# Kernel tuning notes

Measured on AMD Instinct MI355X. Metric: run time of the kernel, lower is better.

Reference implementation:

```python
import jax, jax.numpy as jnp
import numpy as np

BATCH, SEQ, D_IN, D_OUT, PALETTE = 4, 2048, 4096, 4096, 256


def setup_inputs() -> dict:
    key = jax.random.key(0)
    k_in, k_w, k_lut, k_b = jax.random.split(key, 4)
    inp = jax.random.normal(k_in, (BATCH, SEQ, D_IN), dtype=jnp.float32)
    # palette indices playing the role of the stored uint8 weight tensor
    weight = jax.random.randint(k_w, (D_OUT, D_IN), 0, PALETTE, dtype=jnp.int32)
    # fp8-derived palette values (simulated as small fp32 centroids)
    lookup_table = jax.random.normal(k_lut, (PALETTE,), dtype=jnp.float32) * 0.02
    bias = jax.random.normal(k_b, (D_OUT,), dtype=jnp.float32) * 0.01
    return {"input": inp, "lookup_table": lookup_table, "weight": weight, "bias": bias}


def reference(input, lookup_table, weight, bias):
    # Dequantize palette indices -> full weight matrix [D_OUT, D_IN]
    full_weights = lookup_table[weight]
    # F.linear: input @ W^T + bias
    out = jnp.einsum("bsd,od->bso", input, full_weights)
    return out + bias
```

## Files before the change

### kernel.cpp

```cpp
#include <hip/hip_runtime.h>
#include <cstdint>


static constexpr int Md = 8192;
static constexpr int Nd = 4096;
static constexpr int Kd = 4096;
static constexpr int NKT = Kd / 64;

typedef _Float16 half8 __attribute__((ext_vector_type(8)));
typedef float f32x4 __attribute__((ext_vector_type(4)));

__device__ __forceinline__ void async_copy16(const _Float16* g, _Float16* l) {
  __builtin_amdgcn_global_load_lds((const __attribute__((address_space(1))) void*)g,
                                   (__attribute__((address_space(3))) void*)l, 16, 0, 0);
}

__global__ __launch_bounds__(256) void cvt_a(const float* __restrict__ in,
                                             _Float16* __restrict__ out) {
  const size_t i = (size_t)blockIdx.x * 256 + threadIdx.x;
  const float4 x = ((const float4*)in)[2 * i];
  const float4 y = ((const float4*)in)[2 * i + 1];
  half8 h;
  h[0] = (_Float16)x.x; h[1] = (_Float16)x.y; h[2] = (_Float16)x.z; h[3] = (_Float16)x.w;
  h[4] = (_Float16)y.x; h[5] = (_Float16)y.y; h[6] = (_Float16)y.z; h[7] = (_Float16)y.w;
  *(half8*)(out + 8 * i) = h;
}

__global__ __launch_bounds__(256) void dequant_b(const int* __restrict__ w,
                                                 const float* __restrict__ lut,
                                                 _Float16* __restrict__ out) {
  __shared__ float slut[256];
  slut[threadIdx.x] = lut[threadIdx.x];
  __syncthreads();
  const size_t i = (size_t)blockIdx.x * 256 + threadIdx.x;
  const int4 a = ((const int4*)w)[2 * i];
  const int4 b = ((const int4*)w)[2 * i + 1];
  half8 h;
  h[0] = (_Float16)slut[a.x]; h[1] = (_Float16)slut[a.y];
  h[2] = (_Float16)slut[a.z]; h[3] = (_Float16)slut[a.w];
  h[4] = (_Float16)slut[b.x]; h[5] = (_Float16)slut[b.y];
  h[6] = (_Float16)slut[b.z]; h[7] = (_Float16)slut[b.w];
  *(half8*)(out + 8 * i) = h;
}

__global__ __launch_bounds__(512, 2) void gemm_f16(const _Float16* __restrict__ A,
                                                   const _Float16* __restrict__ Bt,
                                                   const float* __restrict__ bias,
                                                   float* __restrict__ C) {
  __shared__ __align__(16) _Float16 As[2][256 * 64];
  __shared__ __align__(16) _Float16 Bs[2][256 * 64];

  const int tid = threadIdx.x;
  const int lane = tid & 63;
  const int wave = tid >> 6;
  const int wm = wave >> 2;
  const int wn = wave & 3;

  const int bid0 = blockIdx.x + blockIdx.y * gridDim.x;
  const int bid = (bid0 & 7) * 64 + (bid0 >> 3);
  const int bm = bid & 31;
  const int bn = bid >> 5;

  const int trow = tid >> 3;
  const int tcol = tid & 7;
  const int gch = tcol ^ (trow & 7);
  const _Float16* ag = A + (size_t)(bm * 256 + trow) * Kd + gch * 8;
  const _Float16* bg = Bt + (size_t)(bn * 256 + trow) * Kd + gch * 8;
  const int lds_off = trow * 64 + tcol * 8;

  auto stage = [&](int buf, int kt) {
#pragma unroll
    for (int ht = 0; ht < 4; ++ht) {
      async_copy16(ag + (size_t)kt * 64 + (size_t)ht * (64 * Kd),
                   &As[buf][lds_off + ht * 4096]);
      async_copy16(bg + (size_t)kt * 64 + (size_t)ht * (64 * Kd),
                   &Bs[buf][lds_off + ht * 4096]);
    }
  };

  const int fr = lane & 15;
  const int fq = lane >> 4;
  const int e = fr & 7;
  const int s0 = (fq ^ e) * 8;
  const int s1 = ((4 | fq) ^ e) * 8;

  f32x4 acc[8][4] = {};

  stage(0, 0);

  for (int kt = 0; kt < NKT; ++kt) {
    const int cur = kt & 1;
    if (kt + 1 < NKT) {
      stage(cur ^ 1, kt + 1);
      asm volatile("s_waitcnt vmcnt(8)" ::: "memory");
    } else {
      asm volatile("s_waitcnt vmcnt(0)" ::: "memory");
    }
    __builtin_amdgcn_s_barrier();

    const _Float16* as = &As[cur][(wm * 128 + fr) * 64];
    const _Float16* bs = &Bs[cur][(wn * 64 + fr) * 64];

    half8 a[4][2], b0[2][2], b1[2][2];

#pragma unroll
    for (int i = 0; i < 4; ++i) {
      a[i][0] = *(const half8*)(as + i * 16 * 64 + s0);
      a[i][1] = *(const half8*)(as + i * 16 * 64 + s1);
    }
#pragma unroll
    for (int j = 0; j < 2; ++j) {
      b0[j][0] = *(const half8*)(bs + j * 16 * 64 + s0);
      b0[j][1] = *(const half8*)(bs + j * 16 * 64 + s1);
    }
    __builtin_amdgcn_s_barrier();
    asm volatile("s_waitcnt lgkmcnt(0)" ::: "memory");
    __builtin_amdgcn_sched_barrier(0);
    __builtin_amdgcn_s_setprio(1);
#pragma unroll
    for (int i = 0; i < 4; ++i)
#pragma unroll
      for (int j = 0; j < 2; ++j) {
        acc[i][j] = __builtin_amdgcn_mfma_f32_16x16x32_f16(a[i][0], b0[j][0], acc[i][j], 0, 0, 0);
        acc[i][j] = __builtin_amdgcn_mfma_f32_16x16x32_f16(a[i][1], b0[j][1], acc[i][j], 0, 0, 0);
      }
    __builtin_amdgcn_s_setprio(0);
    __builtin_amdgcn_s_barrier();

#pragma unroll
    for (int j = 0; j < 2; ++j) {
      b1[j][0] = *(const half8*)(bs + (32 + j * 16) * 64 + s0);
      b1[j][1] = *(const half8*)(bs + (32 + j * 16) * 64 + s1);
    }
    __builtin_amdgcn_s_barrier();
    asm volatile("s_waitcnt lgkmcnt(0)" ::: "memory");
    __builtin_amdgcn_sched_barrier(0);
    __builtin_amdgcn_s_setprio(1);
#pragma unroll
    for (int i = 0; i < 4; ++i)
#pragma unroll
      for (int j = 0; j < 2; ++j) {
        acc[i][2 + j] = __builtin_amdgcn_mfma_f32_16x16x32_f16(a[i][0], b1[j][0], acc[i][2 + j], 0, 0, 0);
        acc[i][2 + j] = __builtin_amdgcn_mfma_f32_16x16x32_f16(a[i][1], b1[j][1], acc[i][2 + j], 0, 0, 0);
      }
    __builtin_amdgcn_s_setprio(0);
    __builtin_amdgcn_s_barrier();

#pragma unroll
    for (int i = 0; i < 4; ++i) {
      a[i][0] = *(const half8*)(as + (64 + i * 16) * 64 + s0);
      a[i][1] = *(const half8*)(as + (64 + i * 16) * 64 + s1);
    }
    __builtin_amdgcn_s_barrier();
    asm volatile("s_waitcnt lgkmcnt(0)" ::: "memory");
    __builtin_amdgcn_sched_barrier(0);
    __builtin_amdgcn_s_setprio(1);
#pragma unroll
    for (int i = 0; i < 4; ++i)
#pragma unroll
      for (int j = 0; j < 2; ++j) {
        acc[4 + i][2 + j] = __builtin_amdgcn_mfma_f32_16x16x32_f16(a[i][0], b1[j][0], acc[4 + i][2 + j], 0, 0, 0);
        acc[4 + i][2 + j] = __builtin_amdgcn_mfma_f32_16x16x32_f16(a[i][1], b1[j][1], acc[4 + i][2 + j], 0, 0, 0);
      }
    __builtin_amdgcn_s_setprio(0);
    __builtin_amdgcn_s_barrier();

    __builtin_amdgcn_s_setprio(1);
#pragma unroll
    for (int i = 0; i < 4; ++i)
#pragma unroll
      for (int j = 0; j < 2; ++j) {
        acc[4 + i][j] = __builtin_amdgcn_mfma_f32_16x16x32_f16(a[i][0], b0[j][0], acc[4 + i][j], 0, 0, 0);
        acc[4 + i][j] = __builtin_amdgcn_mfma_f32_16x16x32_f16(a[i][1], b0[j][1], acc[4 + i][j], 0, 0, 0);
      }
    __builtin_amdgcn_s_setprio(0);
    __builtin_amdgcn_s_barrier();
  }

  const int ccol0 = bn * 256 + wn * 64 + fr;
  const int crow0 = bm * 256 + wm * 128 + fq * 4;
  float bv[4];
#pragma unroll
  for (int j = 0; j < 4; ++j) bv[j] = bias[ccol0 + j * 16];
#pragma unroll
  for (int i = 0; i < 8; ++i) {
#pragma unroll
    for (int r = 0; r < 4; ++r) {
      float* cp = C + (size_t)(crow0 + i * 16 + r) * Nd + ccol0;
#pragma unroll
      for (int j = 0; j < 4; ++j) cp[j * 16] = acc[i][j][r] + bv[j];
    }
  }
}

extern "C" void kernel_launch(void* const* d_in, const int* in_sizes, int n_in,
                              void* d_out, int out_size, void* d_ws, size_t ws_size,
                              hipStream_t stream) {
  const float* inp = (const float*)d_in[0];
  const float* lut = (const float*)d_in[1];
  const int* wgt = (const int*)d_in[2];
  const float* bias = (const float*)d_in[3];
  float* out = (float*)d_out;

  _Float16* Ah = (_Float16*)d_ws;
  _Float16* Bh = (_Float16*)d_ws + (size_t)Md * Kd;

  cvt_a<<<(Md * (size_t)Kd) / (8 * 256), 256, 0, stream>>>(inp, Ah);
  dequant_b<<<((size_t)Nd * Kd) / (8 * 256), 256, 0, stream>>>(wgt, lut, Bh);

  dim3 grid(Md / 256, Nd / 256);
  gemm_f16<<<grid, 512, 0, stream>>>(Ah, Bh, bias, out);
}
```

Baseline: 583.5 us.

## Software-pipeline GEMM main loop with inline-asm LDS reads and fewer barriers

```diff
diff --git a/kernel.cpp b/kernel.cpp
--- a/kernel.cpp
+++ b/kernel.cpp
@@ -14,6 +14,14 @@
   __builtin_amdgcn_global_load_lds((const __attribute__((address_space(1))) void*)g,
                                    (__attribute__((address_space(3))) void*)l, 16, 0, 0);
 }
+
+#define LGKM(n) asm volatile("s_waitcnt lgkmcnt(" #n ")" ::: "memory")
+#define VMCNT(n) asm volatile("s_waitcnt vmcnt(" #n ")" ::: "memory")
+#define BAR() __builtin_amdgcn_s_barrier()
+#define SB0() __builtin_amdgcn_sched_barrier(0)
+
+#define R16(dst, base, OFF) \
+  asm volatile("ds_read_b128 %0, %1 offset:" #OFF : "=v"(dst) : "v"(base))
 
 __global__ __launch_bounds__(256) void cvt_a(const float* __restrict__ in,
                                              _Float16* __restrict__ out) {
@@ -43,7 +51,7 @@
   *(half8*)(out + 8 * i) = h;
 }
 
-__global__ __launch_bounds__(512, 2) void gemm_f16(const _Float16* __restrict__ A,
+__global__ __launch_bounds__(512, 1) void gemm_f16(const _Float16* __restrict__ A,
                                                    const _Float16* __restrict__ Bt,
                                                    const float* __restrict__ bias,
                                                    float* __restrict__ C) {
@@ -81,100 +89,114 @@
   const int fr = lane & 15;
   const int fq = lane >> 4;
   const int e = fr & 7;
-  const int s0 = (fq ^ e) * 8;
-  const int s1 = ((4 | fq) ^ e) * 8;
-
+  const uint32_t aS0 = (uint32_t)(uintptr_t)&As[0][0] +
+                       (uint32_t)((wm * 128 + fr) * 128) + (uint32_t)((fq ^ e) * 16);
+  const uint32_t aS1 = (uint32_t)(uintptr_t)&As[0][0] +
+                       (uint32_t)((wm * 128 + fr) * 128) + (uint32_t)((((4 | fq) ^ e)) * 16);
+  const uint32_t bS0 = (uint32_t)(uintptr_t)&Bs[0][0] +
+                       (uint32_t)((wn * 64 + fr) * 128) + (uint32_t)((fq ^ e) * 16);
+  const uint32_t bS1 = (uint32_t)(uintptr_t)&Bs[0][0] +
+                       (uint32_t)((wn * 64 + fr) * 128) + (uint32_t)((((4 | fq) ^ e)) * 16);
+
+  half8 aL[4][2], aH[4][2], b0A[2][2], b0B[2][2], b1[2][2];
   f32x4 acc[8][4] = {};
 
+#define R_ENTRY_B0()                                             \
+  R16(aL[0][0], aS0, 0);     R16(aL[0][1], aS1, 0);              \
+  R16(aL[1][0], aS0, 2048);  R16(aL[1][1], aS1, 2048);           \
+  R16(aL[2][0], aS0, 4096);  R16(aL[2][1], aS1, 4096);           \
+  R16(aL[3][0], aS0, 6144);  R16(aL[3][1], aS1, 6144);           \
+  R16(b0A[0][0], bS0, 0);    R16(b0A[0][1], bS1, 0);             \
+  R16(b0A[1][0], bS0, 2048); R16(b0A[1][1], bS1, 2048)
+
+#define R_ENTRY_B1()                                             \
+  R16(aL[0][0], aS0, 32768); R16(aL[0][1], aS1, 32768);          \
+  R16(aL[1][0], aS0, 34816); R16(aL[1][1], aS1, 34816);          \
+  R16(aL[2][0], aS0, 36864); R16(aL[2][1], aS1, 36864);          \
+  R16(aL[3][0], aS0, 38912); R16(aL[3][1], aS1, 38912);          \
+  R16(b0B[0][0], bS0, 32768); R16(b0B[0][1], bS1, 32768);        \
+  R16(b0B[1][0], bS0, 34816); R16(b0B[1][1], bS1, 34816)
+
+#define R_B1_0()                                                 \
+  R16(b1[0][0], bS0, 4096);  R16(b1[0][1], bS1, 4096);           \
+  R16(b1[1][0], bS0, 6144);  R16(b1[1][1], bS1, 6144)
+
+#define R_B1_1()                                                 \
+  R16(b1[0][0], bS0, 36864); R16(b1[0][1], bS1, 36864);          \
+  R16(b1[1][0], bS0, 38912); R16(b1[1][1], bS1, 38912)
+
+#define R_AH_0()                                                 \
+  R16(aH[0][0], aS0, 8192);  R16(aH[0][1], aS1, 8192);           \
+  R16(aH[1][0], aS0, 10240); R16(aH[1][1], aS1, 10240);          \
+  R16(aH[2][0], aS0, 12288); R16(aH[2][1], aS1, 12288);          \
+  R16(aH[3][0], aS0, 14336); R16(aH[3][1], aS1, 14336)
+
+#define R_AH_1()                                                 \
+  R16(aH[0][0], aS0, 40960); R16(aH[0][1], aS1, 40960);          \
+  R16(aH[1][0], aS0, 43008); R16(aH[1][1], aS1, 43008);          \
+  R16(aH[2][0], aS0, 45056); R16(aH[2][1], aS1, 45056);          \
+  R16(aH[3][0], aS0, 47104); R16(aH[3][1], aS1, 47104)
+
+#define MF(d, x, y) d = __builtin_amdgcn_mfma_f32_16x16x32_f16(x, y, d, 0, 0, 0)
+
+#define PH0(B0)                                          \
+  _Pragma("unroll") for (int i = 0; i < 4; ++i)          \
+  _Pragma("unroll") for (int j = 0; j < 2; ++j) {        \
+    MF(acc[i][j], aL[i][0], B0[j][0]);                   \
+    MF(acc[i][j], aL[i][1], B0[j][1]);                   \
+  }
+#define PH1()                                            \
+  _Pragma("unroll") for (int i = 0; i < 4; ++i)          \
+  _Pragma("unroll") for (int j = 0; j < 2; ++j) {        \
+    MF(acc[i][2 + j], aL[i][0], b1[j][0]);               \
+    MF(acc[i][2 + j], aL[i][1], b1[j][1]);               \
+  }
+#define PH2()                                            \
+  _Pragma("unroll") for (int i = 0; i < 4; ++i)          \
+  _Pragma("unroll") for (int j = 0; j < 2; ++j) {        \
+    MF(acc[4 + i][2 + j], aH[i][0], b1[j][0]);           \
+    MF(acc[4 + i][2 + j], aH[i][1], b1[j][1]);           \
+  }
+#define PH3(B0)                                          \
+  _Pragma("unroll") for (int i = 0; i < 4; ++i)          \
+  _Pragma("unroll") for (int j = 0; j < 2; ++j) {        \
+    MF(acc[4 + i][j], aH[i][0], B0[j][0]);               \
+    MF(acc[4 + i][j], aH[i][1], B0[j][1]);               \
+  }
+
+#define PRIO1() __builtin_amdgcn_s_setprio(1)
+#define PRIO0() __builtin_amdgcn_s_setprio(0)
+
   stage(0, 0);
-
-  for (int kt = 0; kt < NKT; ++kt) {
-    const int cur = kt & 1;
-    if (kt + 1 < NKT) {
-      stage(cur ^ 1, kt + 1);
-      asm volatile("s_waitcnt vmcnt(8)" ::: "memory");
-    } else {
-      asm volatile("s_waitcnt vmcnt(0)" ::: "memory");
+  stage(1, 1);
+  VMCNT(8);
+  BAR();
+  R_ENTRY_B0();
+
+  for (int kt = 0; kt < NKT; kt += 2) {
+    R_B1_0();
+    LGKM(4); SB0(); PRIO1(); PH0(b0A); PRIO0();
+    R_AH_0();
+    LGKM(8); SB0(); PRIO1(); PH1(); PRIO0();
+    LGKM(0); SB0(); PRIO1(); PH2(); PRIO0();
+    VMCNT(0);
+    BAR();
+    R_ENTRY_B1();
+    if (kt + 2 < NKT) stage(0, kt + 2);
+    SB0(); PRIO1(); PH3(b0A); PRIO0();
+
+    R_B1_1();
+    LGKM(4); SB0(); PRIO1(); PH0(b0B); PRIO0();
+    R_AH_1();
+    LGKM(8); SB0(); PRIO1(); PH1(); PRIO0();
+    LGKM(0); SB0(); PRIO1(); PH2(); PRIO0();
+    VMCNT(0);
+    BAR();
+    if (kt + 2 < NKT) {
+      R_ENTRY_B0();
+      if (kt + 3 < NKT) stage(1, kt + 3);
     }
-    __builtin_amdgcn_s_barrier();
-
-    const _Float16* as = &As[cur][(wm * 128 + fr) * 64];
-    const _Float16* bs = &Bs[cur][(wn * 64 + fr) * 64];
-
-    half8 a[4][2], b0[2][2], b1[2][2];
-
-#pragma unroll
-    for (int i = 0; i < 4; ++i) {
-      a[i][0] = *(const half8*)(as + i * 16 * 64 + s0);
-      a[i][1] = *(const half8*)(as + i * 16 * 64 + s1);
-    }
-#pragma unroll
-    for (int j = 0; j < 2; ++j) {
-      b0[j][0] = *(const half8*)(bs + j * 16 * 64 + s0);
-      b0[j][1] = *(const half8*)(bs + j * 16 * 64 + s1);
-    }
-    __builtin_amdgcn_s_barrier();
-    asm volatile("s_waitcnt lgkmcnt(0)" ::: "memory");
-    __builtin_amdgcn_sched_barrier(0);
-    __builtin_amdgcn_s_setprio(1);
-#pragma unroll
-    for (int i = 0; i < 4; ++i)
-#pragma unroll
-      for (int j = 0; j < 2; ++j) {
-        acc[i][j] = __builtin_amdgcn_mfma_f32_16x16x32_f16(a[i][0], b0[j][0], acc[i][j], 0, 0, 0);
-        acc[i][j] = __builtin_amdgcn_mfma_f32_16x16x32_f16(a[i][1], b0[j][1], acc[i][j], 0, 0, 0);
-      }
-    __builtin_amdgcn_s_setprio(0);
-    __builtin_amdgcn_s_barrier();
-
-#pragma unroll
-    for (int j = 0; j < 2; ++j) {
-      b1[j][0] = *(const half8*)(bs + (32 + j * 16) * 64 + s0);
-      b1[j][1] = *(const half8*)(bs + (32 + j * 16) * 64 + s1);
-    }
-    __builtin_amdgcn_s_barrier();
-    asm volatile("s_waitcnt lgkmcnt(0)" ::: "memory");
-    __builtin_amdgcn_sched_barrier(0);
-    __builtin_amdgcn_s_setprio(1);
-#pragma unroll
-    for (int i = 0; i < 4; ++i)
-#pragma unroll
-      for (int j = 0; j < 2; ++j) {
-        acc[i][2 + j] = __builtin_amdgcn_mfma_f32_16x16x32_f16(a[i][0], b1[j][0], acc[i][2 + j], 0, 0, 0);
-        acc[i][2 + j] = __builtin_amdgcn_mfma_f32_16x16x32_f16(a[i][1], b1[j][1], acc[i][2 + j], 0, 0, 0);
-      }
-    __builtin_amdgcn_s_setprio(0);
-    __builtin_amdgcn_s_barrier();
-
-#pragma unroll
-    for (int i = 0; i < 4; ++i) {
-      a[i][0] = *(const half8*)(as + (64 + i * 16) * 64 + s0);
-      a[i][1] = *(const half8*)(as + (64 + i * 16) * 64 + s1);
-    }
-    __builtin_amdgcn_s_barrier();
-    asm volatile("s_waitcnt lgkmcnt(0)" ::: "memory");
-    __builtin_amdgcn_sched_barrier(0);
-    __builtin_amdgcn_s_setprio(1);
-#pragma unroll
-    for (int i = 0; i < 4; ++i)
-#pragma unroll
-      for (int j = 0; j < 2; ++j) {
-        acc[4 + i][2 + j] = __builtin_amdgcn_mfma_f32_16x16x32_f16(a[i][0], b1[j][0], acc[4 + i][2 + j], 0, 0, 0);
-        acc[4 + i][2 + j] = __builtin_amdgcn_mfma_f32_16x16x32_f16(a[i][1], b1[j][1], acc[4 + i][2 + j], 0, 0, 0);
-      }
-    __builtin_amdgcn_s_setprio(0);
-    __builtin_amdgcn_s_barrier();
-
-    __builtin_amdgcn_s_setprio(1);
-#pragma unroll
-    for (int i = 0; i < 4; ++i)
-#pragma unroll
-      for (int j = 0; j < 2; ++j) {
-        acc[4 + i][j] = __builtin_amdgcn_mfma_f32_16x16x32_f16(a[i][0], b0[j][0], acc[4 + i][j], 0, 0, 0);
-        acc[4 + i][j] = __builtin_amdgcn_mfma_f32_16x16x32_f16(a[i][1], b0[j][1], acc[4 + i][j], 0, 0, 0);
-      }
-    __builtin_amdgcn_s_setprio(0);
-    __builtin_amdgcn_s_barrier();
+    SB0(); PRIO1(); PH3(b0B); PRIO0();
   }
 
   const int ccol0 = bn * 256 + wn * 64 + fr;
```

Result: faster. 497.1 us (-14.8%).
